# Kernel optimization log

Measured on AMD Instinct MI355X. Metric: run time of the kernel, lower is better.

Reference implementation:

```python
import jax, jax.numpy as jnp
import numpy as np

N_HEADS = 16

def _rope(x):
    # x: (B, T, H, D); rotary embedding over sequence positions T
    B, T, H, D = x.shape
    half = D // 2
    freqs = 1.0 / (10000.0 ** (jnp.arange(half, dtype=x.dtype) / half))
    t = jnp.arange(T, dtype=x.dtype)
    ang = t[:, None] * freqs[None, :]            # (T, half)
    cos = jnp.cos(ang)[:, None, :]               # (T, 1, half) broadcast over heads
    sin = jnp.sin(ang)[:, None, :]
    x1, x2 = x[..., :half], x[..., half:]
    return jnp.concatenate([x1 * cos - x2 * sin, x1 * sin + x2 * cos], axis=-1)


def setup_inputs() -> dict:
    key = jax.random.key(0)
    kx, kq, kk, kv, ko = jax.random.split(key, 5)
    B, T, C = 4, 2048, 2048
    x = jax.random.normal(kx, (B, T, C), dtype=jnp.float32)
    # TPLinear (tp_size=1): weight (out_f, in_f), init randn*0.02, no bias
    wq = jax.random.normal(kq, (C, C), dtype=jnp.float32) * 0.02
    wk = jax.random.normal(kk, (C, C), dtype=jnp.float32) * 0.02
    wv = jax.random.normal(kv, (C, C), dtype=jnp.float32) * 0.02
    wo = jax.random.normal(ko, (C, C), dtype=jnp.float32) * 0.02
    return {"x": x, "wq": wq, "wk": wk, "wv": wv, "wo": wo}


def reference(x, wq, wk, wv, wo):
    B, T, C = x.shape
    H = N_HEADS
    D = C // H
    # QKV projections (F.linear: x @ W^T)
    q = (x @ wq.T).reshape(B, T, H, D)
    k = (x @ wk.T).reshape(B, T, H, D)
    v = (x @ wv.T).reshape(B, T, H, D)
    # RoPE on q and k over sequence positions
    q = _rope(q).transpose(0, 2, 1, 3)           # (B, H, T, D)
    k = _rope(k).transpose(0, 2, 1, 3)
    v = v.transpose(0, 2, 1, 3)
    # Causal scaled dot-product attention
    scale = 1.0 / jnp.sqrt(jnp.asarray(D, dtype=x.dtype))
    scores = jnp.einsum("bhqd,bhkd->bhqk", q, k) * scale   # (B, H, T, T)
    causal = jnp.tril(jnp.ones((T, T), dtype=bool))
    scores = jnp.where(causal, scores, jnp.finfo(x.dtype).min)
    att = jax.nn.softmax(scores, axis=-1)
    out = jnp.einsum("bhqk,bhkd->bhqd", att, v)            # (B, H, T, D)
    out = out.transpose(0, 2, 1, 3).reshape(B, T, C)
    return out @ wo.T
```

## Files before the change

kernel.cpp:

```cpp
#include <hip/hip_runtime.h>
#include <hip/hip_bf16.h>
#include <stdint.h>

typedef __hip_bfloat16 bf16;
typedef __bf16 bf16x8_t __attribute__((ext_vector_type(8)));
typedef float f32x4_t __attribute__((ext_vector_type(4)));

#define GAS __attribute__((address_space(1)))
#define LAS __attribute__((address_space(3)))
#define SCHED0 __builtin_amdgcn_sched_barrier(0)

__device__ __forceinline__ f32x4_t mfma16(bf16x8_t a, bf16x8_t b, f32x4_t c) {
    return __builtin_amdgcn_mfma_f32_16x16x32_bf16(a, b, c, 0, 0, 0);
}

__device__ __forceinline__ void gload_lds16(const void* g, void* l) {
    __builtin_amdgcn_global_load_lds((const GAS void*)g, (LAS void*)l, 16, 0, 0);
}

__global__ __launch_bounds__(256) void cast_f32_bf16(const float* __restrict__ in,
                                                     bf16* __restrict__ out, int n4) {
    int stride = gridDim.x * blockDim.x;
    for (int i = blockIdx.x * blockDim.x + threadIdx.x; i < n4; i += stride) {
        float4 f = reinterpret_cast<const float4*>(in)[i];
        bf16 h0 = __float2bfloat16(f.x), h1 = __float2bfloat16(f.y);
        bf16 h2 = __float2bfloat16(f.z), h3 = __float2bfloat16(f.w);
        ushort4 u;
        u.x = *reinterpret_cast<unsigned short*>(&h0);
        u.y = *reinterpret_cast<unsigned short*>(&h1);
        u.z = *reinterpret_cast<unsigned short*>(&h2);
        u.w = *reinterpret_cast<unsigned short*>(&h3);
        reinterpret_cast<ushort4*>(out)[i] = u;
    }
}

__device__ __forceinline__ void store_out(float* p, float v) { *p = v; }
__device__ __forceinline__ void store_out(bf16* p, float v) { *p = __float2bfloat16(v); }

template <typename OutT>
__global__ __launch_bounds__(512, 1) void gemm_nt256(const bf16* __restrict__ A,
                                                     const bf16* __restrict__ B,
                                                     OutT* __restrict__ C,
                                                     int M, int N, int K) {
    __shared__ char lds[131072];
    const int t = threadIdx.x, lane = t & 63, w = t >> 6;
    const int wm = w >> 2, wn = w & 3;
    const int li = lane & 15, hi = lane >> 4, l7 = lane & 7, l3 = lane >> 3;

    const int ny = M >> 8;
    const int cpx = gridDim.x >> 3;
    const int tile = ((int)blockIdx.x & 7) * cpx + ((int)blockIdx.x >> 3);
    const int m0 = (tile % ny) * 256, n0 = (tile / ny) * 256;
    const int NT = K >> 6;

    f32x4_t acc[8][4];
#pragma unroll
    for (int f = 0; f < 8; ++f)
#pragma unroll
        for (int g = 0; g < 4; ++g) acc[f][g] = f32x4_t{0.f, 0.f, 0.f, 0.f};

    bf16x8_t af[2][8], bfr[2][4];

    auto stage = [&](int kt, int p) {
        const char* Ab = (const char*)A;
        const char* Bb = (const char*)B;
        char* la = lds + p * 65536;
        char* lb = la + 32768;
        const int sc = (l7 ^ l3) << 4;
        const size_t kof = (size_t)kt * 128;
#pragma unroll
        for (int c = 0; c < 4; ++c) {
            int row = w * 32 + c * 8 + l3;
            gload_lds16(Ab + (size_t)(m0 + row) * K * 2 + kof + sc,
                        la + (w * 32 + c * 8) * 128);
        }
#pragma unroll
        for (int c = 0; c < 4; ++c) {
            int row = w * 32 + c * 8 + l3;
            gload_lds16(Bb + (size_t)(n0 + row) * K * 2 + kof + sc,
                        lb + (w * 32 + c * 8) * 128);
        }
    };

    auto read_frags = [&](int p) {
        const char* la = lds + p * 65536;
        const char* lb = la + 32768;
#pragma unroll
        for (int kk = 0; kk < 2; ++kk) {
            const int cb = kk * 64 + hi * 16;
#pragma unroll
            for (int f = 0; f < 8; ++f) {
                int r = wm * 128 + f * 16 + li;
                af[kk][f] = *reinterpret_cast<const bf16x8_t*>(
                    la + r * 128 + (cb ^ (l7 << 4)));
            }
#pragma unroll
            for (int g = 0; g < 4; ++g) {
                int r = wn * 64 + g * 16 + li;
                bfr[kk][g] = *reinterpret_cast<const bf16x8_t*>(
                    lb + r * 128 + (cb ^ (l7 << 4)));
            }
        }
    };

    auto do_mfma = [&]() {
        __builtin_amdgcn_s_setprio(1);
#pragma unroll
        for (int kk = 0; kk < 2; ++kk)
#pragma unroll
            for (int f = 0; f < 8; ++f)
#pragma unroll
                for (int g = 0; g < 4; ++g)
                    acc[f][g] = mfma16(af[kk][f], bfr[kk][g], acc[f][g]);
        __builtin_amdgcn_s_setprio(0);
    };

    stage(0, 0);
    stage(1, 1);
    asm volatile("s_waitcnt vmcnt(8)" ::: "memory"); SCHED0;
    __builtin_amdgcn_s_barrier(); SCHED0;

    for (int kt = 0; kt < NT - 2; ++kt) {
        const int p = kt & 1;
        read_frags(p);
        asm volatile("s_waitcnt lgkmcnt(0)" ::: "memory"); SCHED0;
        __builtin_amdgcn_s_barrier(); SCHED0;
        stage(kt + 2, p);
        do_mfma();
        asm volatile("s_waitcnt vmcnt(8)" ::: "memory"); SCHED0;
        __builtin_amdgcn_s_barrier(); SCHED0;
    }
    read_frags((NT - 2) & 1);
    asm volatile("s_waitcnt lgkmcnt(0)" ::: "memory"); SCHED0;
    do_mfma();
    asm volatile("s_waitcnt vmcnt(0)" ::: "memory"); SCHED0;
    __builtin_amdgcn_s_barrier(); SCHED0;
    read_frags((NT - 1) & 1);
    asm volatile("s_waitcnt lgkmcnt(0)" ::: "memory"); SCHED0;
    do_mfma();

#pragma unroll
    for (int f = 0; f < 8; ++f)
#pragma unroll
        for (int g = 0; g < 4; ++g)
#pragma unroll
            for (int r = 0; r < 4; ++r) {
                int row = m0 + wm * 128 + f * 16 + hi * 4 + r;
                int col = n0 + wn * 64 + g * 16 + li;
                store_out(C + (size_t)row * N + col, acc[f][g][r]);
            }
}

__global__ __launch_bounds__(256) void rope_qk(bf16* __restrict__ q, bf16* __restrict__ k,
                                               int total) {
    int idx = blockIdx.x * blockDim.x + threadIdx.x;
    if (idx >= total) return;
    int d = idx & 63;
    int h = (idx >> 6) & 15;
    int bt = idx >> 10;
    int tpos = bt & 2047;
    float freq = expf(-0.14391157f * (float)d);
    float ang = (float)tpos * freq;
    float s, c;
    sincosf(ang, &s, &c);
    size_t base = (size_t)bt * 2048 + h * 128 + d;
    const float scale_q = 0.12751682f;
    {
        float x1 = __bfloat162float(q[base]);
        float x2 = __bfloat162float(q[base + 64]);
        q[base]      = __float2bfloat16((x1 * c - x2 * s) * scale_q);
        q[base + 64] = __float2bfloat16((x1 * s + x2 * c) * scale_q);
    }
    {
        float x1 = __bfloat162float(k[base]);
        float x2 = __bfloat162float(k[base + 64]);
        k[base]      = __float2bfloat16(x1 * c - x2 * s);
        k[base + 64] = __float2bfloat16(x1 * s + x2 * c);
    }
}

__global__ __launch_bounds__(256) void transpose_v(const bf16* __restrict__ v,
                                                   bf16* __restrict__ vT) {
    __shared__ bf16 tile[64][65];
    const int T = 2048, Cc = 2048;
    int bh = blockIdx.z, b = bh >> 4, h = bh & 15;
    int t0 = blockIdx.x * 64, d0 = blockIdx.y * 64;
    int tx = threadIdx.x & 63, ty = threadIdx.x >> 6;
#pragma unroll
    for (int i = 0; i < 16; i++) {
        int tt = ty + i * 4;
        tile[tt][tx] = v[(size_t)(b * T + t0 + tt) * Cc + h * 128 + d0 + tx];
    }
    __syncthreads();
#pragma unroll
    for (int i = 0; i < 16; i++) {
        int dd = ty + i * 4;
        vT[(size_t)(bh * 128 + d0 + dd) * T + t0 + tx] = tile[tx][dd];
    }
}

__global__ __launch_bounds__(256) void flash_attn(const bf16* __restrict__ q,
                                                  const bf16* __restrict__ k,
                                                  const bf16* __restrict__ vT,
                                                  bf16* __restrict__ att) {
    const int T = 2048, Cc = 2048;
    __shared__ bf16 Ks[64 * 128];
    __shared__ bf16 VTs[128 * 64];
    __shared__ bf16 Ps[4][16 * 72];
    const int t = threadIdx.x, lane = t & 63, w = t >> 6;
    const int bh = blockIdx.y, b = bh >> 4, h = bh & 15;
    const int col = lane & 15, hi = lane >> 4;

    for (int pass = 0; pass < 2; ++pass) {
        const int qblk = pass ? (31 - (int)blockIdx.x) : (int)blockIdx.x;
        const int q0 = qblk * 64;

        bf16x8_t qf[4];
        {
            int qrow = q0 + w * 16 + col;
            const char* qb = (const char*)q + ((size_t)(b * T + qrow) * Cc + h * 128) * 2;
#pragma unroll
            for (int kf = 0; kf < 4; kf++)
                qf[kf] = *reinterpret_cast<const bf16x8_t*>(qb + kf * 64 + hi * 16);
        }

        f32x4_t acc[8];
#pragma unroll
        for (int i = 0; i < 8; i++) acc[i] = f32x4_t{0.f, 0.f, 0.f, 0.f};
        float m_run[4] = {-1e30f, -1e30f, -1e30f, -1e30f};
        float l_run[4] = {0.f, 0.f, 0.f, 0.f};

        const int ntiles = qblk + 1;
        for (int ti = 0; ti < ntiles; ++ti) {
            const int k0 = ti * 64;
#pragma unroll
            for (int i = 0; i < 4; ++i) {
                int o = (i * 256 + t) * 16;
                int kr = o >> 8, kc = (o & 255) ^ ((kr & 7) << 4);
                gload_lds16((const char*)k + ((size_t)(b * T + k0 + kr) * Cc + h * 128) * 2 + kc,
                            (char*)Ks + (i * 256 + w * 64) * 16);
                int vr = o >> 7, vc = (o & 127) ^ ((vr & 7) << 4);
                gload_lds16((const char*)vT + ((size_t)(bh * 128 + vr) * T + k0) * 2 + vc,
                            (char*)VTs + (i * 256 + w * 64) * 16);
            }
            __syncthreads();

            f32x4_t s[4];
#pragma unroll
            for (int nb = 0; nb < 4; nb++) {
                s[nb] = f32x4_t{0.f, 0.f, 0.f, 0.f};
#pragma unroll
                for (int kf = 0; kf < 4; kf++) {
                    bf16x8_t kfr = *reinterpret_cast<const bf16x8_t*>(
                        (const char*)Ks + (((nb * 16 + col) * 256 + kf * 64 + hi * 16)
                                           ^ ((col & 7) << 4)));
                    s[nb] = mfma16(qf[kf], kfr, s[nb]);
                }
            }

            const int rowb = q0 + w * 16 + (hi << 2);
            float mt[4] = {-1e30f, -1e30f, -1e30f, -1e30f};
#pragma unroll
            for (int nb = 0; nb < 4; nb++) {
                int kc = k0 + nb * 16 + col;
#pragma unroll
                for (int r = 0; r < 4; r++) {
                    float v = s[nb][r];
                    if (kc > rowb + r) v = -1e30f;
                    s[nb][r] = v;
                    mt[r] = fmaxf(mt[r], v);
                }
            }
#pragma unroll
            for (int r = 0; r < 4; r++) {
#pragma unroll
                for (int mk = 1; mk < 16; mk <<= 1)
                    mt[r] = fmaxf(mt[r], __shfl_xor(mt[r], mk, 64));
            }
            float alpha[4], ls[4];
#pragma unroll
            for (int r = 0; r < 4; r++) {
                float mn = fmaxf(m_run[r], mt[r]);
                alpha[r] = exp2f(m_run[r] - mn);
                m_run[r] = mn;
                ls[r] = 0.f;
            }
#pragma unroll
            for (int nb = 0; nb < 4; nb++)
#pragma unroll
                for (int r = 0; r < 4; r++) {
                    float p = exp2f(s[nb][r] - m_run[r]);
                    s[nb][r] = p;
                    ls[r] += p;
                }
#pragma unroll
            for (int r = 0; r < 4; r++) {
#pragma unroll
                for (int mk = 1; mk < 16; mk <<= 1)
                    ls[r] += __shfl_xor(ls[r], mk, 64);
                l_run[r] = l_run[r] * alpha[r] + ls[r];
            }
#pragma unroll
            for (int i = 0; i < 8; i++)
#pragma unroll
                for (int r = 0; r < 4; r++) acc[i][r] *= alpha[r];

#pragma unroll
            for (int nb = 0; nb < 4; nb++)
#pragma unroll
                for (int r = 0; r < 4; r++)
                    Ps[w][((hi << 2) + r) * 72 + nb * 16 + col] =
                        __float2bfloat16(s[nb][r]);
            asm volatile("s_waitcnt lgkmcnt(0)" ::: "memory");
            __builtin_amdgcn_sched_barrier(0);
            bf16x8_t pf[2];
#pragma unroll
            for (int kb = 0; kb < 2; kb++)
                pf[kb] = *reinterpret_cast<const bf16x8_t*>(
                    (const char*)Ps[w] + col * 144 + kb * 64 + hi * 16);

#pragma unroll
            for (int db = 0; db < 8; db++)
#pragma unroll
                for (int kb = 0; kb < 2; kb++) {
                    bf16x8_t vf = *reinterpret_cast<const bf16x8_t*>(
                        (const char*)VTs + (((db * 16 + col) * 128 + kb * 64 + hi * 16)
                                            ^ ((col & 7) << 4)));
                    acc[db] = mfma16(pf[kb], vf, acc[db]);
                }
            __syncthreads();
        }

#pragma unroll
        for (int r = 0; r < 4; r++) {
            float inv = 1.0f / l_run[r];
            int row = q0 + w * 16 + (hi << 2) + r;
            size_t base = (size_t)(b * T + row) * Cc + h * 128;
#pragma unroll
            for (int db = 0; db < 8; db++)
                att[base + db * 16 + col] = __float2bfloat16(acc[db][r] * inv);
        }
    }
}

extern "C" void kernel_launch(void* const* d_in, const int* in_sizes, int n_in,
                              void* d_out, int out_size, void* d_ws, size_t ws_size,
                              hipStream_t stream) {
    const int B = 4, T = 2048, C = 2048;
    const int M = B * T;
    const float* x  = (const float*)d_in[0];
    const float* wq = (const float*)d_in[1];
    const float* wk = (const float*)d_in[2];
    const float* wv = (const float*)d_in[3];
    const float* wo = (const float*)d_in[4];
    float* out = (float*)d_out;

    char* ws = (char*)d_ws;
    const size_t SZ_X = (size_t)M * C * 2;
    const size_t SZ_W = (size_t)C * C * 2;
    bf16* xb   = (bf16*)(ws);
    bf16* wqb  = (bf16*)(ws + SZ_X);
    bf16* wkb  = (bf16*)(ws + SZ_X + SZ_W);
    bf16* wvb  = (bf16*)(ws + SZ_X + 2 * SZ_W);
    bf16* wob  = (bf16*)(ws + SZ_X + 3 * SZ_W);
    bf16* qb   = (bf16*)(ws + SZ_X + 4 * SZ_W);
    bf16* kb   = (bf16*)(ws + 2 * SZ_X + 4 * SZ_W);
    bf16* vb   = (bf16*)(ws + 3 * SZ_X + 4 * SZ_W);
    bf16* vTb  = (bf16*)(ws + 4 * SZ_X + 4 * SZ_W);
    bf16* attb = (bf16*)(ws + 5 * SZ_X + 4 * SZ_W);

    cast_f32_bf16<<<2048, 256, 0, stream>>>(x, xb, M * C / 4);
    cast_f32_bf16<<<1024, 256, 0, stream>>>(wq, wqb, C * C / 4);
    cast_f32_bf16<<<1024, 256, 0, stream>>>(wk, wkb, C * C / 4);
    cast_f32_bf16<<<1024, 256, 0, stream>>>(wv, wvb, C * C / 4);
    cast_f32_bf16<<<1024, 256, 0, stream>>>(wo, wob, C * C / 4);

    const int nblk = (M / 256) * (C / 256);
    gemm_nt256<bf16><<<nblk, 512, 0, stream>>>(xb, wqb, qb, M, C, C);
    gemm_nt256<bf16><<<nblk, 512, 0, stream>>>(xb, wkb, kb, M, C, C);
    gemm_nt256<bf16><<<nblk, 512, 0, stream>>>(xb, wvb, vb, M, C, C);

    int rope_total = B * T * 16 * 64;
    rope_qk<<<rope_total / 256, 256, 0, stream>>>(qb, kb, rope_total);

    transpose_v<<<dim3(T / 64, 2, B * 16), 256, 0, stream>>>(vb, vTb);

    flash_attn<<<dim3(16, B * 16), 256, 0, stream>>>(qb, kb, vTb, attb);

    gemm_nt256<float><<<nblk, 512, 0, stream>>>(attb, wob, out, M, C, C);
}
```

Measured before the change: 800.2 us.

## Restructure GEMM into 8-wave ping-pong half-tile pipeline and use raw v_exp in attention

Rewrites the GEMM main loop so loads are issued in half-tile chunks interleaved with quarter-tile MFMA groups across two LDS buffers, with barriers between phases. It also raises launch_bounds to two blocks per CU and swaps exp2f for inline v_exp_f32 asm in the attention softmax. The aim is finer overlap of global->LDS loads with MFMA work and cheaper exponentials. In exchange there are many more barriers. With 128KB of LDS per block, two blocks per CU may not fit, so the occupancy hint may only add register pressure. The inline asm also hides the exp from the compiler's scheduler.

New measurement: 712.6 us. -10.9%, faster.

```diff
diff --git a/kernel.cpp b/kernel.cpp
--- a/kernel.cpp
+++ b/kernel.cpp
@@ -16,6 +16,12 @@
 
 __device__ __forceinline__ void gload_lds16(const void* g, void* l) {
     __builtin_amdgcn_global_load_lds((const GAS void*)g, (LAS void*)l, 16, 0, 0);
+}
+
+__device__ __forceinline__ float exp2_fast(float x) {
+    float r;
+    asm volatile("v_exp_f32 %0, %1\n\ts_nop 0" : "=v"(r) : "v"(x));
+    return r;
 }
 
 __global__ __launch_bounds__(256) void cast_f32_bf16(const float* __restrict__ in,
@@ -37,8 +43,46 @@
 __device__ __forceinline__ void store_out(float* p, float v) { *p = v; }
 __device__ __forceinline__ void store_out(bf16* p, float v) { *p = __float2bfloat16(v); }
 
+#define BAR()   do { SCHED0; __builtin_amdgcn_s_barrier(); SCHED0; } while (0)
+#define LGKM0() do { asm volatile("s_waitcnt lgkmcnt(0)" ::: "memory"); SCHED0; } while (0)
+#define VM4()   do { asm volatile("s_waitcnt vmcnt(4)" ::: "memory"); SCHED0; } while (0)
+
+#define READ_A(P, MLO)                                                          \
+    do {                                                                        \
+        const char* la_ = lds + (P) * 65536;                                    \
+        _Pragma("unroll") for (int kk = 0; kk < 2; ++kk)                        \
+        _Pragma("unroll") for (int f = 0; f < 4; ++f) {                         \
+            int r_ = wm * 128 + ((MLO) + f) * 16 + li;                          \
+            af[kk][(MLO) + f] = *reinterpret_cast<const bf16x8_t*>(             \
+                la_ + r_ * 128 + ((kk * 64 + hi * 16) ^ (l7 << 4)));            \
+        }                                                                       \
+    } while (0)
+
+#define READ_B(P, NLO)                                                          \
+    do {                                                                        \
+        const char* lb_ = lds + (P) * 65536 + 32768;                            \
+        _Pragma("unroll") for (int kk = 0; kk < 2; ++kk)                        \
+        _Pragma("unroll") for (int g = 0; g < 2; ++g) {                         \
+            int r_ = wn * 64 + ((NLO) + g) * 16 + li;                           \
+            bfr[kk][(NLO) + g] = *reinterpret_cast<const bf16x8_t*>(            \
+                lb_ + r_ * 128 + ((kk * 64 + hi * 16) ^ (l7 << 4)));            \
+        }                                                                       \
+    } while (0)
+
+#define MFMA_Q(MLO, NLO)                                                        \
+    do {                                                                        \
+        __builtin_amdgcn_s_setprio(1);                                          \
+        _Pragma("unroll") for (int kk = 0; kk < 2; ++kk)                        \
+        _Pragma("unroll") for (int f = 0; f < 4; ++f)                           \
+        _Pragma("unroll") for (int g = 0; g < 2; ++g)                           \
+            acc[(MLO) + f][(NLO) + g] = mfma16(af[kk][(MLO) + f],               \
+                                               bfr[kk][(NLO) + g],              \
+                                               acc[(MLO) + f][(NLO) + g]);      \
+        __builtin_amdgcn_s_setprio(0);                                          \
+    } while (0)
+
 template <typename OutT>
-__global__ __launch_bounds__(512, 1) void gemm_nt256(const bf16* __restrict__ A,
+__global__ __launch_bounds__(512, 2) void gemm_nt256(const bf16* __restrict__ A,
                                                      const bf16* __restrict__ B,
                                                      OutT* __restrict__ C,
                                                      int M, int N, int K) {
@@ -61,83 +105,44 @@
 
     bf16x8_t af[2][8], bfr[2][4];
 
-    auto stage = [&](int kt, int p) {
-        const char* Ab = (const char*)A;
-        const char* Bb = (const char*)B;
-        char* la = lds + p * 65536;
-        char* lb = la + 32768;
+    auto stage_half = [&](int kt, int half, int p) {
+        kt = kt < NT - 1 ? kt : NT - 1;
+        const bf16* src = (half >= 2) ? B : A;
+        const int rb = ((half >= 2) ? n0 : m0) + (half & 1) * 128;
+        char* dst = lds + p * 65536 + (half >= 2 ? 32768 : 0) + (half & 1) * 16384;
         const int sc = (l7 ^ l3) << 4;
-        const size_t kof = (size_t)kt * 128;
-#pragma unroll
-        for (int c = 0; c < 4; ++c) {
-            int row = w * 32 + c * 8 + l3;
-            gload_lds16(Ab + (size_t)(m0 + row) * K * 2 + kof + sc,
-                        la + (w * 32 + c * 8) * 128);
-        }
-#pragma unroll
-        for (int c = 0; c < 4; ++c) {
-            int row = w * 32 + c * 8 + l3;
-            gload_lds16(Bb + (size_t)(n0 + row) * K * 2 + kof + sc,
-                        lb + (w * 32 + c * 8) * 128);
+#pragma unroll
+        for (int l = 0; l < 2; ++l) {
+            int row = rb + l * 64 + w * 8 + l3;
+            gload_lds16((const char*)src + (size_t)row * K * 2 + (size_t)kt * 128 + sc,
+                        dst + (l * 64 + w * 8) * 128);
         }
     };
 
-    auto read_frags = [&](int p) {
-        const char* la = lds + p * 65536;
-        const char* lb = la + 32768;
-#pragma unroll
-        for (int kk = 0; kk < 2; ++kk) {
-            const int cb = kk * 64 + hi * 16;
-#pragma unroll
-            for (int f = 0; f < 8; ++f) {
-                int r = wm * 128 + f * 16 + li;
-                af[kk][f] = *reinterpret_cast<const bf16x8_t*>(
-                    la + r * 128 + (cb ^ (l7 << 4)));
-            }
-#pragma unroll
-            for (int g = 0; g < 4; ++g) {
-                int r = wn * 64 + g * 16 + li;
-                bfr[kk][g] = *reinterpret_cast<const bf16x8_t*>(
-                    lb + r * 128 + (cb ^ (l7 << 4)));
-            }
-        }
-    };
-
-    auto do_mfma = [&]() {
-        __builtin_amdgcn_s_setprio(1);
-#pragma unroll
-        for (int kk = 0; kk < 2; ++kk)
-#pragma unroll
-            for (int f = 0; f < 8; ++f)
-#pragma unroll
-                for (int g = 0; g < 4; ++g)
-                    acc[f][g] = mfma16(af[kk][f], bfr[kk][g], acc[f][g]);
-        __builtin_amdgcn_s_setprio(0);
-    };
-
-    stage(0, 0);
-    stage(1, 1);
-    asm volatile("s_waitcnt vmcnt(8)" ::: "memory"); SCHED0;
-    __builtin_amdgcn_s_barrier(); SCHED0;
-
-    for (int kt = 0; kt < NT - 2; ++kt) {
-        const int p = kt & 1;
-        read_frags(p);
-        asm volatile("s_waitcnt lgkmcnt(0)" ::: "memory"); SCHED0;
-        __builtin_amdgcn_s_barrier(); SCHED0;
-        stage(kt + 2, p);
-        do_mfma();
-        asm volatile("s_waitcnt vmcnt(8)" ::: "memory"); SCHED0;
-        __builtin_amdgcn_s_barrier(); SCHED0;
-    }
-    read_frags((NT - 2) & 1);
-    asm volatile("s_waitcnt lgkmcnt(0)" ::: "memory"); SCHED0;
-    do_mfma();
-    asm volatile("s_waitcnt vmcnt(0)" ::: "memory"); SCHED0;
-    __builtin_amdgcn_s_barrier(); SCHED0;
-    read_frags((NT - 1) & 1);
-    asm volatile("s_waitcnt lgkmcnt(0)" ::: "memory"); SCHED0;
-    do_mfma();
+    stage_half(0, 0, 0); stage_half(0, 1, 0); stage_half(0, 2, 0); stage_half(0, 3, 0);
+    stage_half(1, 0, 1); stage_half(1, 1, 1);
+    VM4(); BAR();
+
+    const int NITER = NT >> 1;
+    for (int j = 0; j < NITER; ++j) {
+        const int t1 = 2 * j + 1;
+        READ_A(0, 0); READ_B(0, 0); stage_half(t1, 2, 1);
+        BAR(); LGKM0(); MFMA_Q(0, 0); BAR();
+        READ_A(0, 4); READ_B(0, 2); stage_half(t1, 3, 1);
+        BAR(); LGKM0(); MFMA_Q(0, 2); BAR();
+        stage_half(t1 + 1, 0, 0);
+        BAR(); MFMA_Q(4, 0); BAR();
+        stage_half(t1 + 1, 1, 0);
+        BAR(); MFMA_Q(4, 2); VM4(); BAR();
+        READ_A(1, 0); READ_B(1, 0); stage_half(t1 + 1, 2, 0);
+        BAR(); LGKM0(); MFMA_Q(0, 0); BAR();
+        READ_A(1, 4); READ_B(1, 2); stage_half(t1 + 1, 3, 0);
+        BAR(); LGKM0(); MFMA_Q(0, 2); BAR();
+        stage_half(t1 + 2, 0, 1);
+        BAR(); MFMA_Q(4, 0); BAR();
+        stage_half(t1 + 2, 1, 1);
+        BAR(); MFMA_Q(4, 2); VM4(); BAR();
+    }
 
 #pragma unroll
     for (int f = 0; f < 8; ++f)
@@ -281,7 +286,7 @@
 #pragma unroll
             for (int r = 0; r < 4; r++) {
                 float mn = fmaxf(m_run[r], mt[r]);
-                alpha[r] = exp2f(m_run[r] - mn);
+                alpha[r] = exp2_fast(m_run[r] - mn);
                 m_run[r] = mn;
                 ls[r] = 0.f;
             }
@@ -289,7 +294,7 @@
             for (int nb = 0; nb < 4; nb++)
 #pragma unroll
                 for (int r = 0; r < 4; r++) {
-                    float p = exp2f(s[nb][r] - m_run[r]);
+                    float p = exp2_fast(s[nb][r] - m_run[r]);
                     s[nb][r] = p;
                     ls[r] += p;
                 }
```
